# Kernel tuning notes

Measured on AMD Instinct MI355X. Metric: run time of the kernel, lower is better.

The kernel has to match this reference:

```python
import jax, jax.numpy as jnp
import numpy as np

MUL = 64      # multiplicity of each irrep (64x0e + 64x1o)
B = 8192      # batch / number of nodes
INV_SQRT3 = float(1.0 / np.sqrt(3.0))  # e3nn wigner_3j normalization for (1,1,0),(0,1,1),(1,0,1)
# component normalization: alpha = sqrt(dim_out / fan_in), fan_in = sum over paths of mul_u*mul_v
FAN_IN = 2 * MUL * MUL  # two paths feed each output irrep
ALPHA0 = float(np.sqrt(1.0 / FAN_IN))  # l_out = 0, dim 1
ALPHA1 = float(np.sqrt(3.0 / FAN_IN))  # l_out = 1, dim 3


def setup_inputs() -> dict:
    key = jax.random.key(0)
    kx, k0, k1, k2, k3 = jax.random.split(key, 5)
    x = jax.random.normal(kx, (B, 4 * MUL), dtype=jnp.float32)  # [B, 64*1 + 64*3]
    w000 = jax.random.normal(k0, (MUL, MUL, MUL), dtype=jnp.float32)  # 0e x 0e -> 0e
    w110 = jax.random.normal(k1, (MUL, MUL, MUL), dtype=jnp.float32)  # 1o x 1o -> 0e
    w011 = jax.random.normal(k2, (MUL, MUL, MUL), dtype=jnp.float32)  # 0e x 1o -> 1o
    w101 = jax.random.normal(k3, (MUL, MUL, MUL), dtype=jnp.float32)  # 1o x 0e -> 1o
    return {"x": x, "w000": w000, "w110": w110, "w011": w011, "w101": w101}


def reference(x, w000, w110, w011, w101):
    # split concatenated irrep features: scalars then vectors
    x0 = x[:, :MUL]                          # [B, U]      l=0 (e)
    x1 = x[:, MUL:].reshape(-1, MUL, 3)      # [B, U, 3]   l=1 (o)

    # path (0e,0e)->0e : CG = 1
    p000 = jnp.einsum('uvw,bu,bv->bw', w000, x0, x0)
    # path (1o,1o)->0e : CG[i,j] = delta_ij / sqrt(3)
    p110 = jnp.einsum('uvw,bui,bvi->bw', w110, x1, x1) * INV_SQRT3
    out0 = ALPHA0 * (p000 + p110)            # [B, W]

    # path (0e,1o)->1o : CG[j,k] = delta_jk / sqrt(3)
    p011 = jnp.einsum('uvw,bu,bvk->bwk', w011, x0, x1) * INV_SQRT3
    # path (1o,0e)->1o : CG[i,k] = delta_ik / sqrt(3)
    p101 = jnp.einsum('uvw,buk,bv->bwk', w101, x1, x0) * INV_SQRT3
    out1 = ALPHA1 * (p011 + p101)            # [B, W, 3]

    return jnp.concatenate([out0, out1.reshape(out1.shape[0], MUL * 3)], axis=-1)
```

## Files before the change

### kernel.cpp

```cpp
#include <hip/hip_runtime.h>
#include <hip/hip_bf16.h>
#include <cstdint>

#define BM 32
#define NTHREADS 640
#define WS_TILE 524288
#define BUF_B 24576
#define SMEM_BYTES (3*BUF_B + 4*64*32*4)

typedef __bf16 bf16x8_t __attribute__((ext_vector_type(8)));
typedef float f32x4_t __attribute__((ext_vector_type(4)));

__device__ __forceinline__ void async_ld16(const void* g, void* l) {
  __builtin_amdgcn_global_load_lds((const __attribute__((address_space(1))) unsigned int*)g,
                                   (__attribute__((address_space(3))) unsigned int*)l,
                                   16, 0, 0);
}

#define SYNC_V4() asm volatile("s_waitcnt vmcnt(4) lgkmcnt(0)\n\ts_barrier" ::: "memory")
#define SYNC_V0() asm volatile("s_waitcnt vmcnt(0) lgkmcnt(0)\n\ts_barrier" ::: "memory")

__global__ __launch_bounds__(256) void prep_weights(const float* __restrict__ w000,
                                                    const float* __restrict__ w110,
                                                    const float* __restrict__ w011,
                                                    const float* __restrict__ w101,
                                                    char* __restrict__ ws) {
  const float A0  = 0.011048543456039806f;
  const float A0I = A0 * 0.57735026918962576f;
  int t = blockIdx.x * 256 + threadIdx.x;
  int u = t >> 9, f = (t >> 6) & 7, l = t & 63;
  int n = f >> 1, kf = f & 1;
  int w = 16 * n + (l & 15);
  int vbase = 8 * (l >> 4) + 32 * kf;
  bf16x8_t p0, p1, pc;
#pragma unroll
  for (int j = 0; j < 8; ++j) {
    int v = vbase + j;
    float a = w000[u * 4096 + v * 64 + w] * A0;
    float b = w110[u * 4096 + v * 64 + w] * A0I;
    float d = (w011[u * 4096 + v * 64 + w] + w101[v * 4096 + u * 64 + w]) * A0;
    p0[j] = (__bf16)a;
    p1[j] = (__bf16)b;
    pc[j] = (__bf16)d;
  }
  int off = u * 8192 + f * 1024 + l * 16;
  *(bf16x8_t*)(ws + off) = p0;
  *(bf16x8_t*)(ws + WS_TILE + off) = p1;
  *(bf16x8_t*)(ws + 2 * WS_TILE + off) = pc;
}

__global__ __launch_bounds__(NTHREADS, 1) void tp_main(const float* __restrict__ x,
                                                       const char* __restrict__ ws,
                                                       float* __restrict__ out) {
  extern __shared__ char smem[];
  float* xS = (float*)(smem + 3 * BUF_B);
  const int tid = threadIdx.x;
  const int wave = tid >> 6, lane = tid & 63;
  const int lr = lane & 15, lg = lane >> 4;
  const int b0 = blockIdx.x * BM;
  const int unit = wave >> 1;
  const int kf = wave & 1;
  const int tsel = (unit == 0) ? 0 : ((unit == 1) ? 1 : 2);

  auto STAGE = [&](int uu, int bufB) {
    if (wave < 6) {
      const char* g = ws + (wave >> 1) * WS_TILE + uu * 8192 + (wave & 1) * 4096 + lane * 16;
      char* l = smem + bufB + (wave >> 1) * 8192 + (wave & 1) * 4096 + lane * 16;
#pragma unroll
      for (int c = 0; c < 4; ++c)
        async_ld16(g + c * 1024, l + c * 1024);
    }
  };

  auto LOADB = [&](bf16x8_t (&bfr)[4], int bufB) {
    const char* wt = smem + bufB + tsel * 8192 + kf * 1024 + lane * 16;
#pragma unroll
    for (int n = 0; n < 4; ++n)
      bfr[n] = *(const bf16x8_t*)(wt + n * 2048);
  };

  STAGE(0, 0);
  STAGE(1, BUF_B);

  for (int idx = tid; idx < 4 * 64 * 32; idx += NTHREADS) {
    int vec = idx >> 11, rem = idx & 2047;
    int uu = rem >> 5, bb = rem & 31;
    int col = (vec == 0) ? uu : (64 + 3 * uu + (vec - 1));
    xS[idx] = x[(b0 + bb) * 256 + col];
  }

  float xp[3][2][8];
  if (unit == 1) {
#pragma unroll
    for (int vi = 0; vi < 3; ++vi)
#pragma unroll
      for (int m = 0; m < 2; ++m)
#pragma unroll
        for (int j = 0; j < 8; ++j) {
          int v = 8 * lg + 32 * kf + j;
          xp[vi][m][j] = x[(b0 + 16 * m + lr) * 256 + 64 + 3 * v + vi];
        }
  } else {
#pragma unroll
    for (int m = 0; m < 2; ++m)
#pragma unroll
      for (int j = 0; j < 8; ++j) {
        int v = 8 * lg + 32 * kf + j;
        int col = (unit == 0) ? v : (64 + 3 * v + (unit - 2));
        xp[0][m][j] = x[(b0 + 16 * m + lr) * 256 + col];
      }
  }

  f32x4_t acc[2][4];
#pragma unroll
  for (int m = 0; m < 2; ++m)
#pragma unroll
    for (int n = 0; n < 4; ++n) {
      f32x4_t z = {0.f, 0.f, 0.f, 0.f};
      acc[m][n] = z;
    }

  auto STEP = [&](bf16x8_t (&bfr)[4], int uu) {
    bf16x8_t afr[2];
    if (unit == 1) {
#pragma unroll
      for (int m = 0; m < 2; ++m) {
        float s0 = xS[1 * 2048 + uu * 32 + 16 * m + lr];
        float s1 = xS[2 * 2048 + uu * 32 + 16 * m + lr];
        float s2 = xS[3 * 2048 + uu * 32 + 16 * m + lr];
#pragma unroll
        for (int j = 0; j < 8; ++j)
          afr[m][j] = (__bf16)(s0 * xp[0][m][j] + s1 * xp[1][m][j] + s2 * xp[2][m][j]);
      }
    } else {
#pragma unroll
      for (int m = 0; m < 2; ++m) {
        float s = xS[uu * 32 + 16 * m + lr];
#pragma unroll
        for (int j = 0; j < 8; ++j)
          afr[m][j] = (__bf16)(s * xp[0][m][j]);
      }
    }
#pragma unroll
    for (int m = 0; m < 2; ++m)
#pragma unroll
      for (int n = 0; n < 4; ++n)
        acc[m][n] = __builtin_amdgcn_mfma_f32_16x16x32_bf16(afr[m], bfr[n], acc[m][n], 0, 0, 0);
  };

  SYNC_V4();

  bf16x8_t bfr[4];
  for (int base = 0; base < 60; base += 3) {
    STAGE(base + 2, 2 * BUF_B);
    LOADB(bfr, 0);
    STEP(bfr, base);
    SYNC_V4();

    STAGE(base + 3, 0);
    LOADB(bfr, BUF_B);
    STEP(bfr, base + 1);
    SYNC_V4();

    STAGE(base + 4, BUF_B);
    LOADB(bfr, 2 * BUF_B);
    STEP(bfr, base + 2);
    SYNC_V4();
  }
  STAGE(62, 2 * BUF_B);
  LOADB(bfr, 0);
  STEP(bfr, 60);
  SYNC_V4();

  STAGE(63, 0);
  LOADB(bfr, BUF_B);
  STEP(bfr, 61);
  SYNC_V4();

  LOADB(bfr, 2 * BUF_B);
  STEP(bfr, 62);
  SYNC_V0();

  LOADB(bfr, 0);
  STEP(bfr, 63);

  __syncthreads();
  float* pscr = (float*)smem;
  if (kf == 1) {
#pragma unroll
    for (int m = 0; m < 2; ++m)
#pragma unroll
      for (int n = 0; n < 4; ++n)
#pragma unroll
        for (int r = 0; r < 4; ++r)
          pscr[unit * 2048 + (16 * m + 4 * lg + r) * 64 + 16 * n + lr] = acc[m][n][r];
  }
  __syncthreads();
  if (kf == 0) {
#pragma unroll
    for (int m = 0; m < 2; ++m)
#pragma unroll
      for (int n = 0; n < 4; ++n)
#pragma unroll
        for (int r = 0; r < 4; ++r)
          acc[m][n][r] += pscr[unit * 2048 + (16 * m + 4 * lg + r) * 64 + 16 * n + lr];
    if (unit == 1) {
#pragma unroll
      for (int m = 0; m < 2; ++m)
#pragma unroll
        for (int n = 0; n < 4; ++n)
#pragma unroll
          for (int r = 0; r < 4; ++r)
            pscr[5 * 2048 + (16 * m + 4 * lg + r) * 64 + 16 * n + lr] = acc[m][n][r];
    }
  }
  __syncthreads();
  if (wave == 0) {
#pragma unroll
    for (int m = 0; m < 2; ++m)
#pragma unroll
      for (int n = 0; n < 4; ++n)
#pragma unroll
        for (int r = 0; r < 4; ++r) {
          int row = 16 * m + 4 * lg + r, col = 16 * n + lr;
          out[(b0 + row) * 256 + col] = acc[m][n][r] + pscr[5 * 2048 + row * 64 + col];
        }
  } else if (kf == 0 && unit >= 2) {
    const int k = unit - 2;
#pragma unroll
    for (int m = 0; m < 2; ++m)
#pragma unroll
      for (int n = 0; n < 4; ++n)
#pragma unroll
        for (int r = 0; r < 4; ++r) {
          int row = 16 * m + 4 * lg + r, col = 16 * n + lr;
          out[(b0 + row) * 256 + 64 + 3 * col + k] = acc[m][n][r];
        }
  }
}

extern "C" void kernel_launch(void* const* d_in, const int* in_sizes, int n_in,
                              void* d_out, int out_size, void* d_ws, size_t ws_size,
                              hipStream_t stream) {
  const float* x    = (const float*)d_in[0];
  const float* w000 = (const float*)d_in[1];
  const float* w110 = (const float*)d_in[2];
  const float* w011 = (const float*)d_in[3];
  const float* w101 = (const float*)d_in[4];
  float* out = (float*)d_out;
  char* ws = (char*)d_ws;

  prep_weights<<<128, 256, 0, stream>>>(w000, w110, w011, w101, ws);

  hipFuncSetAttribute((const void*)tp_main, hipFuncAttributeMaxDynamicSharedMemorySize, SMEM_BYTES);
  tp_main<<<256, NTHREADS, SMEM_BYTES, stream>>>(x, ws, out);
}
```

Baseline: 49.75 us.

## Load weight fragments directly from global into registers, drop LDS staging

Replaces the async global-to-LDS triple-buffered staging of bf16 weight tiles and its per-step barriers with direct per-wave global loads into registers, software-pipelined across three register buffers. This removes 64 block-wide barriers and the LDS round trip. In exchange, waves sharing a weight tile (kf pairs and the two vector units) each fetch it separately from L2, and latency hiding relies on register prefetch depth. Shared memory is re-laid out so the x staging and reduction scratch no longer overlap the weight buffers.

```diff
diff --git a/kernel.cpp b/kernel.cpp
--- a/kernel.cpp
+++ b/kernel.cpp
@@ -5,20 +5,10 @@
 #define BM 32
 #define NTHREADS 640
 #define WS_TILE 524288
-#define BUF_B 24576
-#define SMEM_BYTES (3*BUF_B + 4*64*32*4)
+#define SMEM_BYTES (4*64*32*4 + 6*32*64*4)
 
 typedef __bf16 bf16x8_t __attribute__((ext_vector_type(8)));
 typedef float f32x4_t __attribute__((ext_vector_type(4)));
-
-__device__ __forceinline__ void async_ld16(const void* g, void* l) {
-  __builtin_amdgcn_global_load_lds((const __attribute__((address_space(1))) unsigned int*)g,
-                                   (__attribute__((address_space(3))) unsigned int*)l,
-                                   16, 0, 0);
-}
-
-#define SYNC_V4() asm volatile("s_waitcnt vmcnt(4) lgkmcnt(0)\n\ts_barrier" ::: "memory")
-#define SYNC_V0() asm volatile("s_waitcnt vmcnt(0) lgkmcnt(0)\n\ts_barrier" ::: "memory")
 
 __global__ __launch_bounds__(256) void prep_weights(const float* __restrict__ w000,
                                                     const float* __restrict__ w110,
@@ -53,7 +43,8 @@
                                                        const char* __restrict__ ws,
                                                        float* __restrict__ out) {
   extern __shared__ char smem[];
-  float* xS = (float*)(smem + 3 * BUF_B);
+  float* xS   = (float*)smem;
+  float* pscr = (float*)(smem + 32768);
   const int tid = threadIdx.x;
   const int wave = tid >> 6, lane = tid & 63;
   const int lr = lane & 15, lg = lane >> 4;
@@ -61,26 +52,7 @@
   const int unit = wave >> 1;
   const int kf = wave & 1;
   const int tsel = (unit == 0) ? 0 : ((unit == 1) ? 1 : 2);
-
-  auto STAGE = [&](int uu, int bufB) {
-    if (wave < 6) {
-      const char* g = ws + (wave >> 1) * WS_TILE + uu * 8192 + (wave & 1) * 4096 + lane * 16;
-      char* l = smem + bufB + (wave >> 1) * 8192 + (wave & 1) * 4096 + lane * 16;
-#pragma unroll
-      for (int c = 0; c < 4; ++c)
-        async_ld16(g + c * 1024, l + c * 1024);
-    }
-  };
-
-  auto LOADB = [&](bf16x8_t (&bfr)[4], int bufB) {
-    const char* wt = smem + bufB + tsel * 8192 + kf * 1024 + lane * 16;
-#pragma unroll
-    for (int n = 0; n < 4; ++n)
-      bfr[n] = *(const bf16x8_t*)(wt + n * 2048);
-  };
-
-  STAGE(0, 0);
-  STAGE(1, BUF_B);
+  const char* gw = ws + tsel * WS_TILE + kf * 1024 + lane * 16;
 
   for (int idx = tid; idx < 4 * 64 * 32; idx += NTHREADS) {
     int vec = idx >> 11, rem = idx & 2047;
@@ -120,6 +92,13 @@
       acc[m][n] = z;
     }
 
+  auto LOADG = [&](bf16x8_t (&bfr)[4], int uu) {
+    const char* p = gw + uu * 8192;
+#pragma unroll
+    for (int n = 0; n < 4; ++n)
+      bfr[n] = *(const bf16x8_t*)(p + n * 2048);
+  };
+
   auto STEP = [&](bf16x8_t (&bfr)[4], int uu) {
     bf16x8_t afr[2];
     if (unit == 1) {
@@ -148,44 +127,26 @@
         acc[m][n] = __builtin_amdgcn_mfma_f32_16x16x32_bf16(afr[m], bfr[n], acc[m][n], 0, 0, 0);
   };
 
-  SYNC_V4();
-
-  bf16x8_t bfr[4];
-  for (int base = 0; base < 60; base += 3) {
-    STAGE(base + 2, 2 * BUF_B);
-    LOADB(bfr, 0);
-    STEP(bfr, base);
-    SYNC_V4();
-
-    STAGE(base + 3, 0);
-    LOADB(bfr, BUF_B);
-    STEP(bfr, base + 1);
-    SYNC_V4();
-
-    STAGE(base + 4, BUF_B);
-    LOADB(bfr, 2 * BUF_B);
-    STEP(bfr, base + 2);
-    SYNC_V4();
-  }
-  STAGE(62, 2 * BUF_B);
-  LOADB(bfr, 0);
-  STEP(bfr, 60);
-  SYNC_V4();
-
-  STAGE(63, 0);
-  LOADB(bfr, BUF_B);
-  STEP(bfr, 61);
-  SYNC_V4();
-
-  LOADB(bfr, 2 * BUF_B);
-  STEP(bfr, 62);
-  SYNC_V0();
-
-  LOADB(bfr, 0);
-  STEP(bfr, 63);
-
   __syncthreads();
-  float* pscr = (float*)smem;
+
+  bf16x8_t B0[4], B1[4], B2[4];
+  LOADG(B0, 0);
+  LOADG(B1, 1);
+  for (int u = 0; u < 60; u += 3) {
+    LOADG(B2, u + 2);
+    STEP(B0, u);
+    LOADG(B0, u + 3);
+    STEP(B1, u + 1);
+    LOADG(B1, u + 4);
+    STEP(B2, u + 2);
+  }
+  LOADG(B2, 62);
+  STEP(B0, 60);
+  LOADG(B0, 63);
+  STEP(B1, 61);
+  STEP(B2, 62);
+  STEP(B0, 63);
+
   if (kf == 1) {
 #pragma unroll
     for (int m = 0; m < 2; ++m)
```

Measured after the change: 50.53 us. Within noise of the previous version (+1.6%).
